# Performance work log

Measured on AMD Instinct MI355X. Metric: run time of the kernel, lower is better.

## Reference

```python
import jax, jax.numpy as jnp
import numpy as np

LN_EPS = 1e-5

def _mlp(h, W1, b1, g1, beta1, W2, b2):
    # Linear -> LayerNorm -> SiLU -> Linear (make_mlp with 2 layers, output_activation=None)
    h = h @ W1 + b1
    mu = h.mean(-1, keepdims=True)
    var = h.var(-1, keepdims=True)  # biased var, matches torch LayerNorm
    h = (h - mu) * jax.lax.rsqrt(var + LN_EPS) * g1 + beta1
    h = jax.nn.silu(h)
    return h @ W2 + b2

def setup_inputs() -> dict:
    key = jax.random.key(0)
    ks = jax.random.split(key, 8)
    N, E, H = 50000, 800000, 128
    def init_w(k, fan_in, fan_out):
        lim = 1.0 / np.sqrt(fan_in)
        return jax.random.uniform(k, (fan_in, fan_out), jnp.float32, -lim, lim)
    return {
        "x": jax.random.normal(ks[0], (N, H), jnp.float32),
        "edge_index": jax.random.randint(ks[1], (2, E), 0, N),
        "e": jax.random.normal(ks[2], (E, H), jnp.float32),
        # node network: in 2H (cat of x and sum-aggregated messages)
        "Wn1": init_w(ks[3], 2 * H, H), "bn1": jnp.zeros((H,), jnp.float32),
        "gn1": jnp.ones((H,), jnp.float32), "betan1": jnp.zeros((H,), jnp.float32),
        "Wn2": init_w(ks[4], H, H), "bn2": jnp.zeros((H,), jnp.float32),
        # edge network: in 3H (cat of x_out[start], x_out[end], e)
        "We1": init_w(ks[5], 3 * H, H), "be1": jnp.zeros((H,), jnp.float32),
        "ge1": jnp.ones((H,), jnp.float32), "betae1": jnp.zeros((H,), jnp.float32),
        "We2": init_w(ks[6], H, H), "be2": jnp.zeros((H,), jnp.float32),
    }

def reference(x, edge_index, e, Wn1, bn1, gn1, betan1, Wn2, bn2, We1, be1, ge1, betae1, We2, be2):
    start, end = edge_index[0], edge_index[1]
    # aggregation == 'sum': scatter_add of edge features onto destination nodes
    msgs = jax.ops.segment_sum(e, end, num_segments=x.shape[0])  # [N, H]
    node_inputs = jnp.concatenate([x, msgs], axis=-1)  # [N, 2H]
    x_out = _mlp(node_inputs, Wn1, bn1, gn1, betan1, Wn2, bn2) + x  # residual
    edge_inputs = jnp.concatenate([x_out[start], x_out[end], e], axis=-1)  # [E, 3H]
    e_out = _mlp(edge_inputs, We1, be1, ge1, betae1, We2, be2) + e  # residual
    return (x_out, e_out)
```

## Files before the change

kernel.cpp:

```cpp
#include <hip/hip_runtime.h>

#define H 128
#define LN_EPS 1e-5f

typedef __attribute__((ext_vector_type(8))) short bf16x8;
typedef __attribute__((ext_vector_type(4))) float f32x4;

__device__ __forceinline__ ushort f2bf(float f) {
    unsigned u = __builtin_bit_cast(unsigned, f);
    u += 0x7fffu + ((u >> 16) & 1u);
    return (ushort)(u >> 16);
}

__device__ __forceinline__ float bf2f(ushort u) {
    return __builtin_bit_cast(float, (unsigned)u << 16);
}

__device__ __forceinline__ f32x4 mfma16(bf16x8 a, bf16x8 b, f32x4 c) {
    return __builtin_amdgcn_mfma_f32_16x16x32_bf16(a, b, c, 0, 0, 0);
}

__global__ __launch_bounds__(256) void hist_kernel(
    const int* __restrict__ ei, int* __restrict__ cnt, int E)
{
    int i = blockIdx.x * 256 + threadIdx.x;
    if (i < E) atomicAdd(&cnt[ei[E + i]], 1);
}

__global__ __launch_bounds__(1024) void scan_kernel(
    const int* __restrict__ cnt, int* __restrict__ off,
    int* __restrict__ cursor, int N)
{
    __shared__ int s[1024];
    const int t = threadIdx.x;
    const int chunk = (N + 1023) / 1024;
    const int lo = t * chunk, hi = min(lo + chunk, N);
    int sum = 0;
    for (int i = lo; i < hi; ++i) sum += cnt[i];
    s[t] = sum;
    __syncthreads();
    for (int d = 1; d < 1024; d <<= 1) {
        int v = (t >= d) ? s[t - d] : 0;
        __syncthreads();
        s[t] += v;
        __syncthreads();
    }
    int running = s[t] - sum;
    for (int i = lo; i < hi; ++i) {
        off[i] = running;
        cursor[i] = running;
        running += cnt[i];
    }
    if (t == 1023) off[N] = running;
}

__global__ __launch_bounds__(256) void reorder_kernel(
    const int* __restrict__ ei, int* __restrict__ cursor,
    int* __restrict__ sorted, int E)
{
    int i = blockIdx.x * 256 + threadIdx.x;
    if (i < E) {
        int pos = atomicAdd(&cursor[ei[E + i]], 1);
        sorted[pos] = i;
    }
}

__global__ __launch_bounds__(256) void segsum_kernel(
    const float* __restrict__ e, const int* __restrict__ sorted,
    const int* __restrict__ off, float* __restrict__ msgs, int N)
{
    int node = blockIdx.x * 4 + (threadIdx.x >> 6);
    int lane = threadIdx.x & 63;
    if (node >= N) return;
    int beg = off[node], end = off[node + 1];
    float ax = 0.f, ay = 0.f;
    for (int base = beg; base < end; base += 64) {
        int eid_l = (base + lane < end) ? sorted[base + lane] : 0;
        int cnt = min(64, end - base);
        int i = 0;
        for (; i + 4 <= cnt; i += 4) {
            int e0 = __shfl(eid_l, i), e1 = __shfl(eid_l, i + 1);
            int e2 = __shfl(eid_l, i + 2), e3 = __shfl(eid_l, i + 3);
            float2 v0 = *reinterpret_cast<const float2*>(e + (size_t)e0 * H + lane * 2);
            float2 v1 = *reinterpret_cast<const float2*>(e + (size_t)e1 * H + lane * 2);
            float2 v2 = *reinterpret_cast<const float2*>(e + (size_t)e2 * H + lane * 2);
            float2 v3 = *reinterpret_cast<const float2*>(e + (size_t)e3 * H + lane * 2);
            ax += v0.x + v1.x + v2.x + v3.x;
            ay += v0.y + v1.y + v2.y + v3.y;
        }
        for (; i < cnt; ++i) {
            int eid = __shfl(eid_l, i);
            float2 v = *reinterpret_cast<const float2*>(e + (size_t)eid * H + lane * 2);
            ax += v.x; ay += v.y;
        }
    }
    *reinterpret_cast<float2*>(msgs + (size_t)node * H + lane * 2) = make_float2(ax, ay);
}

__global__ __launch_bounds__(256) void wtrans_kernel(
    const float* __restrict__ W, ushort* __restrict__ Wt, int K)
{
    int idx = blockIdx.x * 256 + threadIdx.x;
    if (idx >= K * H) return;
    int k = idx >> 7, n = idx & (H - 1);
    Wt[n * K + k] = f2bf(W[idx]);
}

__global__ __launch_bounds__(256, 4) void node_mlp_kernel(
    const float* __restrict__ x, const float* __restrict__ msgs,
    const ushort* __restrict__ W1t, const float* __restrict__ b1,
    const float* __restrict__ g1, const float* __restrict__ be1,
    const ushort* __restrict__ W2t, const float* __restrict__ b2,
    float* __restrict__ x_out, ushort* __restrict__ xbf, int N)
{
    __shared__ ushort smem[64 * 264];
    __shared__ float part_s[2][64], part_q[2][64];

    const int tid = threadIdx.x;
    const int row0 = blockIdx.x * 64;

    for (int idx = tid; idx < 64 * 64; idx += 256) {
        int r = idx >> 6, c4 = idx & 63;
        int row = row0 + r;
        float4 v = make_float4(0.f, 0.f, 0.f, 0.f);
        if (row < N)
            v = (c4 < 32) ? reinterpret_cast<const float4*>(x + (size_t)row * H)[c4]
                          : reinterpret_cast<const float4*>(msgs + (size_t)row * H)[c4 - 32];
        ushort4 bv;
        bv.x = f2bf(v.x); bv.y = f2bf(v.y); bv.z = f2bf(v.z); bv.w = f2bf(v.w);
        *reinterpret_cast<ushort4*>(&smem[r * 264 + c4 * 4]) = bv;
    }
    __syncthreads();

    const int lane = tid & 63, w = tid >> 6;
    const int l15 = lane & 15, lg = lane >> 4;
    const int mrow = (w & 1) * 32, ncol = (w >> 1) * 64;

    const ushort* pi0 = smem + (size_t)(mrow + l15) * 264;
    const ushort* pi1 = smem + (size_t)(mrow + 16 + l15) * 264;
    const ushort* pw1 = W1t + (size_t)(ncol + l15) * 256;

    f32x4 acc[2][4];
    #pragma unroll
    for (int mt = 0; mt < 2; ++mt)
        #pragma unroll
        for (int nt = 0; nt < 4; ++nt)
            acc[mt][nt] = (f32x4){0.f, 0.f, 0.f, 0.f};

    #pragma unroll
    for (int ks = 0; ks < 8; ++ks) {
        int k0 = ks * 32 + lg * 8;
        bf16x8 a0 = *reinterpret_cast<const bf16x8*>(pi0 + k0);
        bf16x8 a1 = *reinterpret_cast<const bf16x8*>(pi1 + k0);
        #pragma unroll
        for (int nt = 0; nt < 4; ++nt) {
            bf16x8 bfr = *reinterpret_cast<const bf16x8*>(pw1 + (size_t)nt * 16 * 256 + k0);
            acc[0][nt] = mfma16(a0, bfr, acc[0][nt]);
            acc[1][nt] = mfma16(a1, bfr, acc[1][nt]);
        }
    }

    float b1c[4], g1c[4], be1c[4];
    #pragma unroll
    for (int nt = 0; nt < 4; ++nt) {
        int c = ncol + nt * 16 + l15;
        b1c[nt] = b1[c]; g1c[nt] = g1[c]; be1c[nt] = be1[c];
    }
    #pragma unroll
    for (int mt = 0; mt < 2; ++mt)
        #pragma unroll
        for (int nt = 0; nt < 4; ++nt)
            #pragma unroll
            for (int r = 0; r < 4; ++r)
                acc[mt][nt][r] += b1c[nt];

    #pragma unroll
    for (int mt = 0; mt < 2; ++mt) {
        #pragma unroll
        for (int r = 0; r < 4; ++r) {
            float s = acc[mt][0][r] + acc[mt][1][r] + acc[mt][2][r] + acc[mt][3][r];
            float q = acc[mt][0][r] * acc[mt][0][r] + acc[mt][1][r] * acc[mt][1][r]
                    + acc[mt][2][r] * acc[mt][2][r] + acc[mt][3][r] * acc[mt][3][r];
            #pragma unroll
            for (int m = 8; m >= 1; m >>= 1) {
                s += __shfl_xor(s, m);
                q += __shfl_xor(q, m);
            }
            if (l15 == 0) {
                int rl = mrow + mt * 16 + lg * 4 + r;
                part_s[w >> 1][rl] = s;
                part_q[w >> 1][rl] = q;
            }
        }
    }
    __syncthreads();

    #pragma unroll
    for (int mt = 0; mt < 2; ++mt) {
        #pragma unroll
        for (int r = 0; r < 4; ++r) {
            int rl = mrow + mt * 16 + lg * 4 + r;
            float s  = part_s[0][rl] + part_s[1][rl];
            float q  = part_q[0][rl] + part_q[1][rl];
            float mu = s * (1.0f / H);
            float rs = rsqrtf(q * (1.0f / H) - mu * mu + LN_EPS);
            #pragma unroll
            for (int nt = 0; nt < 4; ++nt) {
                float v = (acc[mt][nt][r] - mu) * rs * g1c[nt] + be1c[nt];
                v = v / (1.0f + __expf(-v));
                smem[rl * 136 + ncol + nt * 16 + l15] = f2bf(v);
            }
        }
    }
    __syncthreads();

    const ushort* ph0 = smem + (size_t)(mrow + l15) * 136;
    const ushort* ph1 = smem + (size_t)(mrow + 16 + l15) * 136;
    const ushort* pw2 = W2t + (size_t)(ncol + l15) * 128;

    f32x4 acc2[2][4];
    #pragma unroll
    for (int nt = 0; nt < 4; ++nt) {
        float bb = b2[ncol + nt * 16 + l15];
        #pragma unroll
        for (int mt = 0; mt < 2; ++mt)
            acc2[mt][nt] = (f32x4){bb, bb, bb, bb};
    }
    #pragma unroll
    for (int ks = 0; ks < 4; ++ks) {
        int k0 = ks * 32 + lg * 8;
        bf16x8 a0 = *reinterpret_cast<const bf16x8*>(ph0 + k0);
        bf16x8 a1 = *reinterpret_cast<const bf16x8*>(ph1 + k0);
        #pragma unroll
        for (int nt = 0; nt < 4; ++nt) {
            bf16x8 bfr = *reinterpret_cast<const bf16x8*>(pw2 + (size_t)nt * 16 * 128 + k0);
            acc2[0][nt] = mfma16(a0, bfr, acc2[0][nt]);
            acc2[1][nt] = mfma16(a1, bfr, acc2[1][nt]);
        }
    }

    #pragma unroll
    for (int mt = 0; mt < 2; ++mt) {
        #pragma unroll
        for (int r = 0; r < 4; ++r) {
            int row = row0 + mrow + mt * 16 + lg * 4 + r;
            if (row < N) {
                const float* rp = x + (size_t)row * H;
                float* op = x_out + (size_t)row * H;
                ushort* bp = xbf + (size_t)row * H;
                #pragma unroll
                for (int nt = 0; nt < 4; ++nt) {
                    int c = ncol + nt * 16 + l15;
                    float o = acc2[mt][nt][r] + rp[c];
                    op[c] = o;
                    bp[c] = f2bf(o);
                }
            }
        }
    }
}

__global__ __launch_bounds__(256, 4) void pmat_kernel(
    const ushort* __restrict__ xbf, const ushort* __restrict__ W1t,
    ushort* __restrict__ Pa, ushort* __restrict__ Pb, int N)
{
    __shared__ ushort xs[64 * 136];

    const int tid = threadIdx.x;
    const int row0 = blockIdx.x * 64;

    for (int idx = tid; idx < 64 * 16; idx += 256) {
        int r = idx >> 4, c = idx & 15;
        int row = min(row0 + r, N - 1);
        *reinterpret_cast<bf16x8*>(&xs[r * 136 + c * 8]) =
            *reinterpret_cast<const bf16x8*>(xbf + (size_t)row * H + c * 8);
    }
    __syncthreads();

    const int lane = tid & 63, w = tid >> 6;
    const int l15 = lane & 15, lg = lane >> 4;
    const int mrow = (w & 1) * 32, ncol = (w >> 1) * 64;
    const int rA0 = mrow + l15, rA1 = mrow + 16 + l15;

    const ushort* px0 = xs + (size_t)rA0 * 136 + lg * 8;
    const ushort* px1 = xs + (size_t)rA1 * 136 + lg * 8;
    const ushort* pwa = W1t + (size_t)(ncol + l15) * 384 + lg * 8;
    const ushort* pwb = pwa + 128;

    f32x4 aa[2][4], ab[2][4];
    #pragma unroll
    for (int mt = 0; mt < 2; ++mt)
        #pragma unroll
        for (int nt = 0; nt < 4; ++nt) {
            aa[mt][nt] = (f32x4){0.f, 0.f, 0.f, 0.f};
            ab[mt][nt] = (f32x4){0.f, 0.f, 0.f, 0.f};
        }

    #pragma unroll
    for (int t = 0; t < 4; ++t) {
        bf16x8 a0 = *reinterpret_cast<const bf16x8*>(px0 + t * 32);
        bf16x8 a1 = *reinterpret_cast<const bf16x8*>(px1 + t * 32);
        #pragma unroll
        for (int nt = 0; nt < 4; ++nt) {
            bf16x8 ba = *reinterpret_cast<const bf16x8*>(pwa + (size_t)nt * 16 * 384 + t * 32);
            bf16x8 bb = *reinterpret_cast<const bf16x8*>(pwb + (size_t)nt * 16 * 384 + t * 32);
            aa[0][nt] = mfma16(a0, ba, aa[0][nt]);
            aa[1][nt] = mfma16(a1, ba, aa[1][nt]);
            ab[0][nt] = mfma16(a0, bb, ab[0][nt]);
            ab[1][nt] = mfma16(a1, bb, ab[1][nt]);
        }
    }

    #pragma unroll
    for (int mt = 0; mt < 2; ++mt) {
        #pragma unroll
        for (int r = 0; r < 4; ++r) {
            int row = row0 + mrow + mt * 16 + lg * 4 + r;
            if (row < N) {
                ushort* pa = Pa + (size_t)row * H;
                ushort* pb = Pb + (size_t)row * H;
                #pragma unroll
                for (int nt = 0; nt < 4; ++nt) {
                    int c = ncol + nt * 16 + l15;
                    pa[c] = f2bf(aa[mt][nt][r]);
                    pb[c] = f2bf(ab[mt][nt][r]);
                }
            }
        }
    }
}

__global__ __launch_bounds__(256, 4) void edge_mlp_kernel(
    const ushort* __restrict__ Pa, const ushort* __restrict__ Pb,
    const float* __restrict__ e, const int* __restrict__ ei,
    const ushort* __restrict__ W1t,
    const float* __restrict__ b1,
    const float* __restrict__ g1, const float* __restrict__ be1,
    const ushort* __restrict__ W2t, const float* __restrict__ b2,
    float* __restrict__ e_out, int E)
{
    __shared__ ushort es[64 * 136];
    __shared__ ushort ps[64 * 136];
    __shared__ float part_s[2][64], part_q[2][64];

    const int tid = threadIdx.x;
    const int row0 = blockIdx.x * 64;

    for (int idx = tid; idx < 64 * 16; idx += 256) {
        int r = idx >> 4, c = idx & 15;
        int rr = min(row0 + r, E - 1);
        int s = ei[rr], d = ei[E + rr];
        bf16x8 va = *reinterpret_cast<const bf16x8*>(Pa + (size_t)s * H + c * 8);
        bf16x8 vb = *reinterpret_cast<const bf16x8*>(Pb + (size_t)d * H + c * 8);
        bf16x8 o;
        #pragma unroll
        for (int j = 0; j < 8; ++j)
            o[j] = (short)f2bf(bf2f((ushort)va[j]) + bf2f((ushort)vb[j]));
        *reinterpret_cast<bf16x8*>(&ps[r * 136 + c * 8]) = o;
    }

    for (int idx = tid; idx < 64 * 32; idx += 256) {
        int r = idx >> 5, c4 = idx & 31;
        int row = row0 + r;
        float4 v = make_float4(0.f, 0.f, 0.f, 0.f);
        if (row < E)
            v = reinterpret_cast<const float4*>(e + (size_t)row * H)[c4];
        ushort4 bv;
        bv.x = f2bf(v.x); bv.y = f2bf(v.y); bv.z = f2bf(v.z); bv.w = f2bf(v.w);
        *reinterpret_cast<ushort4*>(&es[r * 136 + c4 * 4]) = bv;
    }
    __syncthreads();

    const int lane = tid & 63, w = tid >> 6;
    const int l15 = lane & 15, lg = lane >> 4;
    const int mrow = (w & 1) * 32, ncol = (w >> 1) * 64;
    const int rA0 = mrow + l15, rA1 = mrow + 16 + l15;

    const ushort* pe0 = es + (size_t)rA0 * 136 + lg * 8;
    const ushort* pe1 = es + (size_t)rA1 * 136 + lg * 8;
    const ushort* pw1 = W1t + (size_t)(ncol + l15) * 384 + 256 + lg * 8;

    f32x4 acc[2][4];
    #pragma unroll
    for (int mt = 0; mt < 2; ++mt)
        #pragma unroll
        for (int nt = 0; nt < 4; ++nt)
            acc[mt][nt] = (f32x4){0.f, 0.f, 0.f, 0.f};

    #pragma unroll
    for (int t = 0; t < 4; ++t) {
        bf16x8 a0 = *reinterpret_cast<const bf16x8*>(pe0 + t * 32);
        bf16x8 a1 = *reinterpret_cast<const bf16x8*>(pe1 + t * 32);
        #pragma unroll
        for (int nt = 0; nt < 4; ++nt) {
            bf16x8 bfr = *reinterpret_cast<const bf16x8*>(pw1 + (size_t)nt * 16 * 384 + t * 32);
            acc[0][nt] = mfma16(a0, bfr, acc[0][nt]);
            acc[1][nt] = mfma16(a1, bfr, acc[1][nt]);
        }
    }

    float b1c[4], g1c[4], be1c[4];
    #pragma unroll
    for (int nt = 0; nt < 4; ++nt) {
        int c = ncol + nt * 16 + l15;
        b1c[nt] = b1[c]; g1c[nt] = g1[c]; be1c[nt] = be1[c];
    }
    #pragma unroll
    for (int mt = 0; mt < 2; ++mt)
        #pragma unroll
        for (int r = 0; r < 4; ++r) {
            int rl = mrow + mt * 16 + lg * 4 + r;
            #pragma unroll
            for (int nt = 0; nt < 4; ++nt)
                acc[mt][nt][r] += b1c[nt] + bf2f(ps[rl * 136 + ncol + nt * 16 + l15]);
        }

    #pragma unroll
    for (int mt = 0; mt < 2; ++mt) {
        #pragma unroll
        for (int r = 0; r < 4; ++r) {
            float s = acc[mt][0][r] + acc[mt][1][r] + acc[mt][2][r] + acc[mt][3][r];
            float q = acc[mt][0][r] * acc[mt][0][r] + acc[mt][1][r] * acc[mt][1][r]
                    + acc[mt][2][r] * acc[mt][2][r] + acc[mt][3][r] * acc[mt][3][r];
            #pragma unroll
            for (int m = 8; m >= 1; m >>= 1) {
                s += __shfl_xor(s, m);
                q += __shfl_xor(q, m);
            }
            if (l15 == 0) {
                int rl = mrow + mt * 16 + lg * 4 + r;
                part_s[w >> 1][rl] = s;
                part_q[w >> 1][rl] = q;
            }
        }
    }
    __syncthreads();

    #pragma unroll
    for (int mt = 0; mt < 2; ++mt) {
        #pragma unroll
        for (int r = 0; r < 4; ++r) {
            int rl = mrow + mt * 16 + lg * 4 + r;
            float s  = part_s[0][rl] + part_s[1][rl];
            float q  = part_q[0][rl] + part_q[1][rl];
            float mu = s * (1.0f / H);
            float rs = rsqrtf(q * (1.0f / H) - mu * mu + LN_EPS);
            #pragma unroll
            for (int nt = 0; nt < 4; ++nt) {
                float v = (acc[mt][nt][r] - mu) * rs * g1c[nt] + be1c[nt];
                v = v / (1.0f + __expf(-v));
                es[rl * 136 + ncol + nt * 16 + l15] = f2bf(v);
            }
        }
    }
    __syncthreads();

    const ushort* ph0 = es + (size_t)rA0 * 136;
    const ushort* ph1 = es + (size_t)rA1 * 136;
    const ushort* pw2 = W2t + (size_t)(ncol + l15) * 128;

    f32x4 acc2[2][4];
    #pragma unroll
    for (int nt = 0; nt < 4; ++nt) {
        float bb = b2[ncol + nt * 16 + l15];
        #pragma unroll
        for (int mt = 0; mt < 2; ++mt)
            acc2[mt][nt] = (f32x4){bb, bb, bb, bb};
    }
    #pragma unroll
    for (int ks = 0; ks < 4; ++ks) {
        int k0 = ks * 32 + lg * 8;
        bf16x8 a0 = *reinterpret_cast<const bf16x8*>(ph0 + k0);
        bf16x8 a1 = *reinterpret_cast<const bf16x8*>(ph1 + k0);
        #pragma unroll
        for (int nt = 0; nt < 4; ++nt) {
            bf16x8 bfr = *reinterpret_cast<const bf16x8*>(pw2 + (size_t)nt * 16 * 128 + k0);
            acc2[0][nt] = mfma16(a0, bfr, acc2[0][nt]);
            acc2[1][nt] = mfma16(a1, bfr, acc2[1][nt]);
        }
    }

    #pragma unroll
    for (int mt = 0; mt < 2; ++mt) {
        #pragma unroll
        for (int r = 0; r < 4; ++r) {
            int row = row0 + mrow + mt * 16 + lg * 4 + r;
            if (row < E) {
                const float* rp = e + (size_t)row * H;
                float* op = e_out + (size_t)row * H;
                #pragma unroll
                for (int nt = 0; nt < 4; ++nt) {
                    int c = ncol + nt * 16 + l15;
                    op[c] = acc2[mt][nt][r] + rp[c];
                }
            }
        }
    }
}

extern "C" void kernel_launch(void* const* d_in, const int* in_sizes, int n_in,
                              void* d_out, int out_size, void* d_ws, size_t ws_size,
                              hipStream_t stream)
{
    const float* x     = (const float*)d_in[0];
    const int*   ei    = (const int*)  d_in[1];
    const float* e     = (const float*)d_in[2];
    const float* Wn1   = (const float*)d_in[3];
    const float* bn1   = (const float*)d_in[4];
    const float* gn1   = (const float*)d_in[5];
    const float* betan1= (const float*)d_in[6];
    const float* Wn2   = (const float*)d_in[7];
    const float* bn2   = (const float*)d_in[8];
    const float* We1   = (const float*)d_in[9];
    const float* be1   = (const float*)d_in[10];
    const float* ge1   = (const float*)d_in[11];
    const float* betae1= (const float*)d_in[12];
    const float* We2   = (const float*)d_in[13];
    const float* be2   = (const float*)d_in[14];

    const int N = in_sizes[0] / H;
    const int E = in_sizes[2] / H;

    float* x_out = (float*)d_out;
    float* e_out = (float*)d_out + (long long)N * H;

    char* p = (char*)d_ws;
    float*  msgs = (float*)p;            p += (size_t)N * H * sizeof(float);
    ushort* xbf  = (ushort*)p;           p += (size_t)N * H * sizeof(ushort);
    ushort* Pa   = (ushort*)p;           p += (size_t)N * H * sizeof(ushort);
    ushort* Pb   = (ushort*)p;           p += (size_t)N * H * sizeof(ushort);
    ushort* Wn1t = (ushort*)p;           p += (size_t)256 * H * sizeof(ushort);
    ushort* Wn2t = (ushort*)p;           p += (size_t)H * H * sizeof(ushort);
    ushort* We1t = (ushort*)p;           p += (size_t)384 * H * sizeof(ushort);
    ushort* We2t = (ushort*)p;           p += (size_t)H * H * sizeof(ushort);
    p = (char*)(((size_t)p + 15) & ~(size_t)15);
    int* cnt    = (int*)p;               p += (size_t)N * sizeof(int);
    int* off    = (int*)p;               p += ((size_t)N + 1) * sizeof(int);
    int* cursor = (int*)p;               p += (size_t)N * sizeof(int);
    int* sorted = (int*)p;               p += (size_t)E * sizeof(int);

    wtrans_kernel<<<(256 * H + 255) / 256, 256, 0, stream>>>(Wn1, Wn1t, 256);
    wtrans_kernel<<<(H * H + 255) / 256, 256, 0, stream>>>(Wn2, Wn2t, H);
    wtrans_kernel<<<(384 * H + 255) / 256, 256, 0, stream>>>(We1, We1t, 384);
    wtrans_kernel<<<(H * H + 255) / 256, 256, 0, stream>>>(We2, We2t, H);

    hipMemsetAsync(cnt, 0, (size_t)N * sizeof(int), stream);
    hist_kernel<<<(E + 255) / 256, 256, 0, stream>>>(ei, cnt, E);
    scan_kernel<<<1, 1024, 0, stream>>>(cnt, off, cursor, N);
    reorder_kernel<<<(E + 255) / 256, 256, 0, stream>>>(ei, cursor, sorted, E);
    segsum_kernel<<<(N + 3) / 4, 256, 0, stream>>>(e, sorted, off, msgs, N);

    {
        int blocks = (N + 63) / 64;
        node_mlp_kernel<<<blocks, 256, 0, stream>>>(
            x, msgs, Wn1t, bn1, gn1, betan1, Wn2t, bn2, x_out, xbf, N);
    }
    {
        int blocks = (N + 63) / 64;
        pmat_kernel<<<blocks, 256, 0, stream>>>(xbf, We1t, Pa, Pb, N);
    }
    {
        int blocks = (E + 63) / 64;
        edge_mlp_kernel<<<blocks, 256, 0, stream>>>(
            Pa, Pb, e, ei, We1t, be1, ge1, betae1, We2t, be2, e_out, E);
    }
}
```

Baseline: 758.4 us.

## Fuse Pa/Pb projection into node MLP and use packed bf16 conversion

Merges the separate pmat kernel into the node MLP kernel. The residual output is kept in registers, staged as bf16 in shared memory, and immediately multiplied by the edge W1 slices to produce Pa/Pb. This removes the xbf round trip through global memory and one kernel launch. It also replaces scalar round-to-nearest bf16 conversion with the packed v_cvt_pk_bf16_f32 instruction in the staging loops. The launch bound is lowered to 3 blocks per CU to make room for the extra registers, which may reduce occupancy.

```diff
diff --git a/kernel.cpp b/kernel.cpp
--- a/kernel.cpp
+++ b/kernel.cpp
@@ -14,6 +14,12 @@
 
 __device__ __forceinline__ float bf2f(ushort u) {
     return __builtin_bit_cast(float, (unsigned)u << 16);
+}
+
+__device__ __forceinline__ unsigned cvt_pk(float lo, float hi) {
+    unsigned r;
+    asm("v_cvt_pk_bf16_f32 %0, %1, %2" : "=v"(r) : "v"(lo), "v"(hi));
+    return r;
 }
 
 __device__ __forceinline__ f32x4 mfma16(bf16x8 a, bf16x8 b, f32x4 c) {
@@ -106,12 +112,14 @@
     Wt[n * K + k] = f2bf(W[idx]);
 }
 
-__global__ __launch_bounds__(256, 4) void node_mlp_kernel(
+__global__ __launch_bounds__(256, 3) void node_mlp_kernel(
     const float* __restrict__ x, const float* __restrict__ msgs,
     const ushort* __restrict__ W1t, const float* __restrict__ b1,
     const float* __restrict__ g1, const float* __restrict__ be1,
     const ushort* __restrict__ W2t, const float* __restrict__ b2,
-    float* __restrict__ x_out, ushort* __restrict__ xbf, int N)
+    const ushort* __restrict__ We1t,
+    float* __restrict__ x_out,
+    ushort* __restrict__ Pa, ushort* __restrict__ Pb, int N)
 {
     __shared__ ushort smem[64 * 264];
     __shared__ float part_s[2][64], part_q[2][64];
@@ -126,18 +134,18 @@
         if (row < N)
             v = (c4 < 32) ? reinterpret_cast<const float4*>(x + (size_t)row * H)[c4]
                           : reinterpret_cast<const float4*>(msgs + (size_t)row * H)[c4 - 32];
-        ushort4 bv;
-        bv.x = f2bf(v.x); bv.y = f2bf(v.y); bv.z = f2bf(v.z); bv.w = f2bf(v.w);
-        *reinterpret_cast<ushort4*>(&smem[r * 264 + c4 * 4]) = bv;
+        uint2 pk = make_uint2(cvt_pk(v.x, v.y), cvt_pk(v.z, v.w));
+        *reinterpret_cast<uint2*>(&smem[r * 264 + c4 * 4]) = pk;
     }
     __syncthreads();
 
     const int lane = tid & 63, w = tid >> 6;
     const int l15 = lane & 15, lg = lane >> 4;
     const int mrow = (w & 1) * 32, ncol = (w >> 1) * 64;
-
-    const ushort* pi0 = smem + (size_t)(mrow + l15) * 264;
-    const ushort* pi1 = smem + (size_t)(mrow + 16 + l15) * 264;
+    const int rA0 = mrow + l15, rA1 = mrow + 16 + l15;
+
+    const ushort* pi0 = smem + (size_t)rA0 * 264;
+    const ushort* pi1 = smem + (size_t)rA1 * 264;
     const ushort* pw1 = W1t + (size_t)(ncol + l15) * 256;
 
     f32x4 acc[2][4];
@@ -214,8 +222,8 @@
     }
     __syncthreads();
 
-    const ushort* ph0 = smem + (size_t)(mrow + l15) * 136;
-    const ushort* ph1 = smem + (size_t)(mrow + 16 + l15) * 136;
+    const ushort* ph0 = smem + (size_t)rA0 * 136;
+    const ushort* ph1 = smem + (size_t)rA1 * 136;
     const ushort* pw2 = W2t + (size_t)(ncol + l15) * 128;
 
     f32x4 acc2[2][4];
@@ -247,44 +255,33 @@
             if (row < N) {
                 const float* rp = x + (size_t)row * H;
                 float* op = x_out + (size_t)row * H;
-                ushort* bp = xbf + (size_t)row * H;
                 #pragma unroll
                 for (int nt = 0; nt < 4; ++nt) {
                     int c = ncol + nt * 16 + l15;
                     float o = acc2[mt][nt][r] + rp[c];
                     op[c] = o;
-                    bp[c] = f2bf(o);
+                    acc2[mt][nt][r] = o;
                 }
             }
         }
     }
-}
-
-__global__ __launch_bounds__(256, 4) void pmat_kernel(
-    const ushort* __restrict__ xbf, const ushort* __restrict__ W1t,
-    ushort* __restrict__ Pa, ushort* __restrict__ Pb, int N)
-{
-    __shared__ ushort xs[64 * 136];
-
-    const int tid = threadIdx.x;
-    const int row0 = blockIdx.x * 64;
-
-    for (int idx = tid; idx < 64 * 16; idx += 256) {
-        int r = idx >> 4, c = idx & 15;
-        int row = min(row0 + r, N - 1);
-        *reinterpret_cast<bf16x8*>(&xs[r * 136 + c * 8]) =
-            *reinterpret_cast<const bf16x8*>(xbf + (size_t)row * H + c * 8);
-    }
-    __syncthreads();
-
-    const int lane = tid & 63, w = tid >> 6;
-    const int l15 = lane & 15, lg = lane >> 4;
-    const int mrow = (w & 1) * 32, ncol = (w >> 1) * 64;
-    const int rA0 = mrow + l15, rA1 = mrow + 16 + l15;
-
-    const ushort* px0 = xs + (size_t)rA0 * 136 + lg * 8;
-    const ushort* px1 = xs + (size_t)rA1 * 136 + lg * 8;
-    const ushort* pwa = W1t + (size_t)(ncol + l15) * 384 + lg * 8;
+    __syncthreads();
+
+    #pragma unroll
+    for (int mt = 0; mt < 2; ++mt) {
+        #pragma unroll
+        for (int r = 0; r < 4; ++r) {
+            int rl = mrow + mt * 16 + lg * 4 + r;
+            #pragma unroll
+            for (int nt = 0; nt < 4; ++nt)
+                smem[rl * 136 + ncol + nt * 16 + l15] = f2bf(acc2[mt][nt][r]);
+        }
+    }
+    __syncthreads();
+
+    const ushort* px0 = smem + (size_t)rA0 * 136 + lg * 8;
+    const ushort* px1 = smem + (size_t)rA1 * 136 + lg * 8;
+    const ushort* pwa = We1t + (size_t)(ncol + l15) * 384 + lg * 8;
     const ushort* pwb = pwa + 128;
 
     f32x4 aa[2][4], ab[2][4];
@@ -352,11 +349,17 @@
         int s = ei[rr], d = ei[E + rr];
         bf16x8 va = *reinterpret_cast<const bf16x8*>(Pa + (size_t)s * H + c * 8);
         bf16x8 vb = *reinterpret_cast<const bf16x8*>(Pb + (size_t)d * H + c * 8);
-        bf16x8 o;
-        #pragma unroll
-        for (int j = 0; j < 8; ++j)
-            o[j] = (short)f2bf(bf2f((ushort)va[j]) + bf2f((ushort)vb[j]));
-        *reinterpret_cast<bf16x8*>(&ps[r * 136 + c * 8]) = o;
+        float f0 = bf2f((ushort)va[0]) + bf2f((ushort)vb[0]);
+        float f1 = bf2f((ushort)va[1]) + bf2f((ushort)vb[1]);
+        float f2 = bf2f((ushort)va[2]) + bf2f((ushort)vb[2]);
+        float f3 = bf2f((ushort)va[3]) + bf2f((ushort)vb[3]);
+        float f4 = bf2f((ushort)va[4]) + bf2f((ushort)vb[4]);
+        float f5 = bf2f((ushort)va[5]) + bf2f((ushort)vb[5]);
+        float f6 = bf2f((ushort)va[6]) + bf2f((ushort)vb[6]);
+        float f7 = bf2f((ushort)va[7]) + bf2f((ushort)vb[7]);
+        uint4 pk = make_uint4(cvt_pk(f0, f1), cvt_pk(f2, f3),
+                              cvt_pk(f4, f5), cvt_pk(f6, f7));
+        *reinterpret_cast<uint4*>(&ps[r * 136 + c * 8]) = pk;
     }
 
     for (int idx = tid; idx < 64 * 32; idx += 256) {
@@ -365,9 +368,8 @@
         float4 v = make_float4(0.f, 0.f, 0.f, 0.f);
         if (row < E)
             v = reinterpret_cast<const float4*>(e + (size_t)row * H)[c4];
-        ushort4 bv;
-        bv.x = f2bf(v.x); bv.y = f2bf(v.y); bv.z = f2bf(v.z); bv.w = f2bf(v.w);
-        *reinterpret_cast<ushort4*>(&es[r * 136 + c4 * 4]) = bv;
+        uint2 pk = make_uint2(cvt_pk(v.x, v.y), cvt_pk(v.z, v.w));
+        *reinterpret_cast<uint2*>(&es[r * 136 + c4 * 4]) = pk;
     }
     __syncthreads();
 
@@ -526,7 +528,6 @@
 
     char* p = (char*)d_ws;
     float*  msgs = (float*)p;            p += (size_t)N * H * sizeof(float);
-    ushort* xbf  = (ushort*)p;           p += (size_t)N * H * sizeof(ushort);
     ushort* Pa   = (ushort*)p;           p += (size_t)N * H * sizeof(ushort);
     ushort* Pb   = (ushort*)p;           p += (size_t)N * H * sizeof(ushort);
     ushort* Wn1t = (ushort*)p;           p += (size_t)256 * H * sizeof(ushort);
@@ -553,11 +554,8 @@
     {
         int blocks = (N + 63) / 64;
         node_mlp_kernel<<<blocks, 256, 0, stream>>>(
-            x, msgs, Wn1t, bn1, gn1, betan1, Wn2t, bn2, x_out, xbf, N);
-    }
-    {
-        int blocks = (N + 63) / 64;
-        pmat_kernel<<<blocks, 256, 0, stream>>>(xbf, We1t, Pa, Pb, N);
+            x, msgs, Wn1t, bn1, gn1, betan1, Wn2t, bn2, We1t,
+            x_out, Pa, Pb, N);
     }
     {
         int blocks = (E + 63) / 64;
```

Result: no change. 761.4 us (+0.4%).
